# Optimization experiments

Hardware: AMD Instinct MI355X
Metric: run time of the kernel (lower is better)

Reference implementation:

```python
import jax, jax.numpy as jnp
import numpy as np

EPS = 1e-7   # keras.backend.epsilon() added before log in ctc_batch_cost
NEG = -1e30  # log-space 'zero'

B, T, C, L = 256, 1024, 96, 64


def setup_inputs() -> dict:
    key = jax.random.key(0)
    k1, k2 = jax.random.split(key)
    y_true = jax.random.randint(k1, (B, L), 0, C - 1, dtype=jnp.int32)  # labels in [0, C-2], blank = C-1
    y_pred = jax.random.uniform(k2, (B, T, C), dtype=jnp.float32)
    y_pred = y_pred / jnp.sum(y_pred, axis=-1, keepdims=True)  # valid softmax-like probabilities
    return {"y_true": y_true, "y_pred": y_pred}


def _ctc_loss(y_pred, y_true):
    # Faithful re-implementation of keras.backend.ctc_batch_cost with
    # input_length = T and label_length = L for every batch row.
    b, t, c = y_pred.shape
    l = y_true.shape[1]
    blank = c - 1
    s = 2 * l + 1  # extended label length (blanks interleaved)

    logp = jnp.log(y_pred + EPS)  # [B, T, C]

    # extended label sequence: blank, l0, blank, l1, ..., blank
    ext = jnp.full((b, s), blank, dtype=y_true.dtype).at[:, 1::2].set(y_true)  # [B, S]

    # emission log-probs per (t, b, s)
    lp = jnp.take_along_axis(logp, jnp.broadcast_to(ext[:, None, :], (b, t, s)), axis=2)  # [B, T, S]
    lp = jnp.transpose(lp, (1, 0, 2))  # [T, B, S]

    # skip transition s-2 -> s allowed iff ext[s] != blank and ext[s] != ext[s-2]
    ext_m2 = jnp.pad(ext, ((0, 0), (2, 0)), constant_values=-1)[:, :s]
    skip_ok = (ext != blank) & (ext != ext_m2)  # [B, S]

    alpha0 = jnp.full((b, s), NEG, dtype=logp.dtype)
    alpha0 = alpha0.at[:, 0].set(lp[0, :, 0]).at[:, 1].set(lp[0, :, 1])

    def step(alpha, lp_t):
        a1 = jnp.pad(alpha, ((0, 0), (1, 0)), constant_values=NEG)[:, :s]
        a2 = jnp.pad(alpha, ((0, 0), (2, 0)), constant_values=NEG)[:, :s]
        a2 = jnp.where(skip_ok, a2, NEG)
        new = jax.nn.logsumexp(jnp.stack([alpha, a1, a2]), axis=0) + lp_t
        return new, None

    alpha, _ = jax.lax.scan(step, alpha0, lp[1:])

    loss = -jax.nn.logsumexp(jnp.stack([alpha[:, s - 1], alpha[:, s - 2]]), axis=0)
    return loss[:, None]  # [B, 1], matching ctc_batch_cost


def reference(y_true, y_pred):
    return _ctc_loss(y_pred, y_true)
```

## Files before the change

kernel.cpp:

```cpp
#include <hip/hip_runtime.h>
#include <cstdint>


constexpr int BB = 256;
constexpr int TT = 1024;
constexpr int CC = 96;
constexpr int LL = 64;
#define EPSF 1e-7f

__device__ __forceinline__ float wf_shr1_f(float v) {
  int r = __builtin_amdgcn_update_dpp(0, __float_as_int(v), 0x138 , 0xF, 0xF, false);
  return __int_as_float(r);
}

template <int CTRL>
__device__ __forceinline__ float dpp_max(float v) {
  int r = __builtin_amdgcn_update_dpp(__float_as_int(v), __float_as_int(v), CTRL, 0xF, 0xF, false);
  return fmaxf(v, __int_as_float(r));
}

#define GL(dst, ptr, OFF)                                              \
  asm volatile("global_load_dword %0, %1, off offset:" #OFF            \
               : "=&v"(dst) : "v"(ptr))

#define ISSUE(s) do {                                                  \
    GL(Pl[s][0], ql, 0);    GL(Pl[s][1], ql, 384);                     \
    GL(Pl[s][2], ql, 768);  GL(Pl[s][3], ql, 1152);                    \
    GL(Pl[s][4], ql, 1536); GL(Pl[s][5], ql, 1920);                    \
    GL(Pl[s][6], ql, 2304); GL(Pl[s][7], ql, 2688);                    \
    GL(Pb[s][0], qb, 0);    GL(Pb[s][1], qb, 384);                     \
    GL(Pb[s][2], qb, 768);  GL(Pb[s][3], qb, 1152);                    \
    GL(Pb[s][4], qb, 1536); GL(Pb[s][5], qb, 1920);                    \
    GL(Pb[s][6], qb, 2304); GL(Pb[s][7], qb, 2688);                    \
    ql += 8 * CC; qb += 8 * CC;                                        \
  } while (0)

#define WAITN(N) do {                                                  \
    asm volatile("s_waitcnt vmcnt(" #N ")" ::: "memory");              \
    __builtin_amdgcn_sched_barrier(0);                                 \
  } while (0)

#define STEP8(s) do {                                                  \
    _Pragma("unroll")                                                  \
    for (int u = 0; u < 8; ++u) {                                      \
      const float PL  = Pl[s][u] + EPSF;                               \
      const float PB  = Pb[s][u] + EPSF;                               \
      const float a1p = wf_shr1_f(a1);                \
      const float na0 = (a0 + a1p) * PB;              \
      const float na2 = (a2 + a1) * PB;               \
      const float na1 = fmaf(a1p, mskip, a1 + a0) * PL;      \
      a0 = na0; a1 = na1; a2 = na2;                                    \
    }                                                                  \
  } while (0)

#define RESCALE do {                                                   \
    float m = fmaxf(fmaxf(a0, a1), a2);                                \
    m = dpp_max<0x111>(m);                             \
    m = dpp_max<0x112>(m);                             \
    m = dpp_max<0x114>(m);                             \
    m = dpp_max<0x118>(m);                             \
    m = dpp_max<0x142>(m);                           \
    m = dpp_max<0x143>(m);      \
    const int mb = __builtin_amdgcn_readlane(__float_as_int(m), 63);   \
    const int k  = 223 - ((mb >> 23) & 0xFF);        \
    scale += k;                                                        \
    a0 = ldexpf(a0, k); a1 = ldexpf(a1, k); a2 = ldexpf(a2, k);        \
  } while (0)

__global__ void __launch_bounds__(64, 1)
ctc_fwd(const int* __restrict__ y_true, const float* __restrict__ y_pred,
        float* __restrict__ out) {
  const int b    = blockIdx.x;
  const int lane = threadIdx.x;

  const int lab  = y_true[b * LL + lane];
  const int labp = __builtin_amdgcn_update_dpp(-1, lab, 0x138, 0xF, 0xF, false);
  const float mskip = (lane > 0 && lab != labp) ? 1.0f : 0.0f;

  const float* __restrict__ p = y_pred + (size_t)b * (TT * CC);
  const float* ql = p + lab;
  const float* qb = p + (CC - 1);

  float Pl[4][8], Pb[4][8];

  float a0 = (lane == 0) ? 1.0f : 0.0f;
  float a1 = 0.0f;
  float a2 = 0.0f;
  int   scale = 0;

  ISSUE(0); ISSUE(1); ISSUE(2);

#pragma unroll 1
  for (int it = 0; it < 31; ++it) {
    WAITN(32); ISSUE(3); STEP8(0);
    WAITN(32); ISSUE(0); STEP8(1); RESCALE;
    WAITN(32); ISSUE(1); STEP8(2);
    WAITN(32); ISSUE(2); STEP8(3); RESCALE;
  }
  WAITN(32); ISSUE(3); STEP8(0);
  WAITN(32);           STEP8(1); RESCALE;
  WAITN(16);           STEP8(2);
  WAITN(0);            STEP8(3); RESCALE;

  if (lane == 63) {
    const float s = a1 + a2;
    out[b] = 0.693147180559945f * ((float)scale - log2f(s));
  }
}

extern "C" void kernel_launch(void* const* d_in, const int* in_sizes, int n_in,
                              void* d_out, int out_size, void* d_ws, size_t ws_size,
                              hipStream_t stream) {
  (void)in_sizes; (void)n_in; (void)d_ws; (void)ws_size; (void)out_size;
  const int*   y_true = (const int*)d_in[0];
  const float* y_pred = (const float*)d_in[1];
  float*       out    = (float*)d_out;
  ctc_fwd<<<BB, 64, 0, stream>>>(y_true, y_pred, out);
}
```

Baseline: 155.1 us.

## Repack gathered emissions into bf16 coalesced workspace before serial CTC scan

A new parallel pre-pass kernel gathers each lane's label probability and the blank probability per timestep, rounds them to bf16, and writes them in a lane-contiguous layout to the workspace. The serial scan kernel then reads them with wide dwordx4 loads instead of sixteen scattered dword loads per eight steps, shortening the latency-bound per-step memory path. This adds a second launch and a full pass over y_pred, and bf16 rounding reduces probability precision, which may shift the loss slightly. The original kernel is kept as a fallback when the workspace is too small.

```diff
diff --git a/kernel.cpp b/kernel.cpp
--- a/kernel.cpp
+++ b/kernel.cpp
@@ -8,6 +8,8 @@
 constexpr int LL = 64;
 #define EPSF 1e-7f
 
+typedef __attribute__((ext_vector_type(4))) int i32x4;
+
 __device__ __forceinline__ float wf_shr1_f(float v) {
   int r = __builtin_amdgcn_update_dpp(0, __float_as_int(v), 0x138 , 0xF, 0xF, false);
   return __int_as_float(r);
@@ -19,32 +21,74 @@
   return fmaxf(v, __int_as_float(r));
 }
 
-#define GL(dst, ptr, OFF)                                              \
-  asm volatile("global_load_dword %0, %1, off offset:" #OFF            \
+__device__ __forceinline__ unsigned f2bf(float f) {
+  unsigned x = __float_as_uint(f);
+  return (x + 0x7fffu + ((x >> 16) & 1u)) >> 16;
+}
+
+__global__ void __launch_bounds__(256)
+ctc_repack(const int* __restrict__ y_true, const float* __restrict__ y_pred,
+           unsigned* __restrict__ Lout , ushort* __restrict__ Bout) {
+  __shared__ alignas(16) float tile[64 * CC];
+  __shared__ int labs[64];
+  const int blk = blockIdx.x;
+  const int b   = blk >> 4;
+  const int t0  = (blk & 15) * 64;
+  const int tid = threadIdx.x;
+
+  if (tid < 64) labs[tid] = y_true[b * LL + tid];
+  const float* src = y_pred + ((size_t)b * TT + t0) * CC;
+#pragma unroll
+  for (int j = 0; j < 6; ++j)
+    reinterpret_cast<float4*>(tile)[j * 256 + tid] =
+        reinterpret_cast<const float4*>(src)[j * 256 + tid];
+  __syncthreads();
+
+  const int i   = tid & 63;
+  const int gp  = tid >> 6;
+  const int lab = labs[i];
+#pragma unroll
+  for (int k = 0; k < 2; ++k) {
+    const int gl = gp * 2 + k;
+    unsigned o0, o1, o2, o3;
+    {
+      unsigned a, c;
+      a = f2bf(tile[(gl * 8 + 0) * CC + lab]); c = f2bf(tile[(gl * 8 + 1) * CC + lab]); o0 = a | (c << 16);
+      a = f2bf(tile[(gl * 8 + 2) * CC + lab]); c = f2bf(tile[(gl * 8 + 3) * CC + lab]); o1 = a | (c << 16);
+      a = f2bf(tile[(gl * 8 + 4) * CC + lab]); c = f2bf(tile[(gl * 8 + 5) * CC + lab]); o2 = a | (c << 16);
+      a = f2bf(tile[(gl * 8 + 6) * CC + lab]); c = f2bf(tile[(gl * 8 + 7) * CC + lab]); o3 = a | (c << 16);
+    }
+    const int g = b * 128 + (t0 >> 3) + gl;
+    reinterpret_cast<uint4*>(Lout)[(size_t)g * 64 + i] = make_uint4(o0, o1, o2, o3);
+  }
+  if (tid < 64) Bout[(size_t)b * TT + t0 + tid] = (ushort)f2bf(tile[tid * CC + (CC - 1)]);
+}
+
+#define GLX4(dst, ptr, OFF)                                            \
+  asm volatile("global_load_dwordx4 %0, %1, off offset:" #OFF          \
                : "=&v"(dst) : "v"(ptr))
-
-#define ISSUE(s) do {                                                  \
-    GL(Pl[s][0], ql, 0);    GL(Pl[s][1], ql, 384);                     \
-    GL(Pl[s][2], ql, 768);  GL(Pl[s][3], ql, 1152);                    \
-    GL(Pl[s][4], ql, 1536); GL(Pl[s][5], ql, 1920);                    \
-    GL(Pl[s][6], ql, 2304); GL(Pl[s][7], ql, 2688);                    \
-    GL(Pb[s][0], qb, 0);    GL(Pb[s][1], qb, 384);                     \
-    GL(Pb[s][2], qb, 768);  GL(Pb[s][3], qb, 1152);                    \
-    GL(Pb[s][4], qb, 1536); GL(Pb[s][5], qb, 1920);                    \
-    GL(Pb[s][6], qb, 2304); GL(Pb[s][7], qb, 2688);                    \
-    ql += 8 * CC; qb += 8 * CC;                                        \
-  } while (0)
 
 #define WAITN(N) do {                                                  \
     asm volatile("s_waitcnt vmcnt(" #N ")" ::: "memory");              \
     __builtin_amdgcn_sched_barrier(0);                                 \
   } while (0)
 
+#define ISSUE(s, OFF, BOFF) do {                                       \
+    GLX4(Lv[s], ql, OFF);                                              \
+    GLX4(Bv[s], qb, BOFF);                                             \
+  } while (0)
+
+#define ADV do { ql += 4096; qb += 64; } while (0)
+
 #define STEP8(s) do {                                                  \
     _Pragma("unroll")                                                  \
     for (int u = 0; u < 8; ++u) {                                      \
-      const float PL  = Pl[s][u] + EPSF;                               \
-      const float PB  = Pb[s][u] + EPSF;                               \
+      const int ld = Lv[s][u >> 1];                                    \
+      const int bd = Bv[s][u >> 1];                                    \
+      const int li = (u & 1) ? (ld & 0xffff0000) : (ld << 16);         \
+      const int bi = (u & 1) ? (bd & 0xffff0000) : (bd << 16);         \
+      const float PL  = __int_as_float(li) + EPSF;                     \
+      const float PB  = __int_as_float(bi) + EPSF;                     \
       const float a1p = wf_shr1_f(a1);                \
       const float na0 = (a0 + a1p) * PB;              \
       const float na2 = (a2 + a1) * PB;               \
@@ -55,16 +99,81 @@
 
 #define RESCALE do {                                                   \
     float m = fmaxf(fmaxf(a0, a1), a2);                                \
-    m = dpp_max<0x111>(m);                             \
-    m = dpp_max<0x112>(m);                             \
-    m = dpp_max<0x114>(m);                             \
-    m = dpp_max<0x118>(m);                             \
-    m = dpp_max<0x142>(m);                           \
-    m = dpp_max<0x143>(m);      \
+    m = dpp_max<0x111>(m); m = dpp_max<0x112>(m);                      \
+    m = dpp_max<0x114>(m); m = dpp_max<0x118>(m);                      \
+    m = dpp_max<0x142>(m); m = dpp_max<0x143>(m);                      \
     const int mb = __builtin_amdgcn_readlane(__float_as_int(m), 63);   \
     const int k  = 223 - ((mb >> 23) & 0xFF);        \
     scale += k;                                                        \
     a0 = ldexpf(a0, k); a1 = ldexpf(a1, k); a2 = ldexpf(a2, k);        \
+  } while (0)
+
+__global__ void __launch_bounds__(64, 1)
+ctc_scan(const int* __restrict__ y_true, const unsigned* __restrict__ Lin,
+         const ushort* __restrict__ Bin, float* __restrict__ out) {
+  const int b    = blockIdx.x;
+  const int lane = threadIdx.x;
+
+  const int lab  = y_true[b * LL + lane];
+  const int labp = __builtin_amdgcn_update_dpp(-1, lab, 0x138, 0xF, 0xF, false);
+  const float mskip = (lane > 0 && lab != labp) ? 1.0f : 0.0f;
+
+  const char* ql = (const char*)Lin + (size_t)b * 131072 + lane * 16;
+  const char* qb = (const char*)Bin + (size_t)b * 2048;
+
+  i32x4 Lv[4], Bv[4];
+  float a0 = (lane == 0) ? 1.0f : 0.0f;
+  float a1 = 0.0f, a2 = 0.0f;
+  int scale = 0;
+
+  ISSUE(0, 0, 0); ISSUE(1, 1024, 16); ISSUE(2, 2048, 32);
+
+#pragma unroll 1
+  for (int it = 0; it < 31; ++it) {
+    WAITN(4); ISSUE(3, 3072, 48); STEP8(0);
+    ADV;
+    WAITN(4); ISSUE(0, 0, 0);     STEP8(1); RESCALE;
+    WAITN(4); ISSUE(1, 1024, 16); STEP8(2);
+    WAITN(4); ISSUE(2, 2048, 32); STEP8(3); RESCALE;
+  }
+  WAITN(4); ISSUE(3, 3072, 48); STEP8(0);
+  WAITN(4);                      STEP8(1); RESCALE;
+  WAITN(2);                      STEP8(2);
+  WAITN(0);                      STEP8(3); RESCALE;
+
+  if (lane == 63) {
+    const float s = a1 + a2;
+    out[b] = 0.693147180559945f * ((float)scale - log2f(s));
+  }
+}
+
+#define GL(dst, ptr, OFF)                                              \
+  asm volatile("global_load_dword %0, %1, off offset:" #OFF            \
+               : "=&v"(dst) : "v"(ptr))
+
+#define FISSUE(s) do {                                                 \
+    GL(Pl[s][0], fql, 0);    GL(Pl[s][1], fql, 384);                   \
+    GL(Pl[s][2], fql, 768);  GL(Pl[s][3], fql, 1152);                  \
+    GL(Pl[s][4], fql, 1536); GL(Pl[s][5], fql, 1920);                  \
+    GL(Pl[s][6], fql, 2304); GL(Pl[s][7], fql, 2688);                  \
+    GL(Pb[s][0], fqb, 0);    GL(Pb[s][1], fqb, 384);                   \
+    GL(Pb[s][2], fqb, 768);  GL(Pb[s][3], fqb, 1152);                  \
+    GL(Pb[s][4], fqb, 1536); GL(Pb[s][5], fqb, 1920);                  \
+    GL(Pb[s][6], fqb, 2304); GL(Pb[s][7], fqb, 2688);                  \
+    fql += 8 * CC; fqb += 8 * CC;                                      \
+  } while (0)
+
+#define FSTEP8(s) do {                                                 \
+    _Pragma("unroll")                                                  \
+    for (int u = 0; u < 8; ++u) {                                      \
+      const float PL  = Pl[s][u] + EPSF;                               \
+      const float PB  = Pb[s][u] + EPSF;                               \
+      const float a1p = wf_shr1_f(a1);                                 \
+      const float na0 = (a0 + a1p) * PB;                               \
+      const float na2 = (a2 + a1) * PB;                                \
+      const float na1 = fmaf(a1p, mskip, a1 + a0) * PL;                \
+      a0 = na0; a1 = na1; a2 = na2;                                    \
+    }                                                                  \
   } while (0)
 
 __global__ void __launch_bounds__(64, 1)
@@ -72,36 +181,28 @@
         float* __restrict__ out) {
   const int b    = blockIdx.x;
   const int lane = threadIdx.x;
-
   const int lab  = y_true[b * LL + lane];
   const int labp = __builtin_amdgcn_update_dpp(-1, lab, 0x138, 0xF, 0xF, false);
   const float mskip = (lane > 0 && lab != labp) ? 1.0f : 0.0f;
-
   const float* __restrict__ p = y_pred + (size_t)b * (TT * CC);
-  const float* ql = p + lab;
-  const float* qb = p + (CC - 1);
-
+  const float* fql = p + lab;
+  const float* fqb = p + (CC - 1);
   float Pl[4][8], Pb[4][8];
-
   float a0 = (lane == 0) ? 1.0f : 0.0f;
-  float a1 = 0.0f;
-  float a2 = 0.0f;
-  int   scale = 0;
-
-  ISSUE(0); ISSUE(1); ISSUE(2);
-
+  float a1 = 0.0f, a2 = 0.0f;
+  int scale = 0;
+  FISSUE(0); FISSUE(1); FISSUE(2);
 #pragma unroll 1
   for (int it = 0; it < 31; ++it) {
-    WAITN(32); ISSUE(3); STEP8(0);
-    WAITN(32); ISSUE(0); STEP8(1); RESCALE;
-    WAITN(32); ISSUE(1); STEP8(2);
-    WAITN(32); ISSUE(2); STEP8(3); RESCALE;
-  }
-  WAITN(32); ISSUE(3); STEP8(0);
-  WAITN(32);           STEP8(1); RESCALE;
-  WAITN(16);           STEP8(2);
-  WAITN(0);            STEP8(3); RESCALE;
-
+    WAITN(32); FISSUE(3); FSTEP8(0);
+    WAITN(32); FISSUE(0); FSTEP8(1); RESCALE;
+    WAITN(32); FISSUE(1); FSTEP8(2);
+    WAITN(32); FISSUE(2); FSTEP8(3); RESCALE;
+  }
+  WAITN(32); FISSUE(3); FSTEP8(0);
+  WAITN(32);            FSTEP8(1); RESCALE;
+  WAITN(16);            FSTEP8(2);
+  WAITN(0);             FSTEP8(3); RESCALE;
   if (lane == 63) {
     const float s = a1 + a2;
     out[b] = 0.693147180559945f * ((float)scale - log2f(s));
@@ -111,9 +212,19 @@
 extern "C" void kernel_launch(void* const* d_in, const int* in_sizes, int n_in,
                               void* d_out, int out_size, void* d_ws, size_t ws_size,
                               hipStream_t stream) {
-  (void)in_sizes; (void)n_in; (void)d_ws; (void)ws_size; (void)out_size;
+  (void)in_sizes; (void)n_in; (void)out_size;
   const int*   y_true = (const int*)d_in[0];
   const float* y_pred = (const float*)d_in[1];
   float*       out    = (float*)d_out;
-  ctc_fwd<<<BB, 64, 0, stream>>>(y_true, y_pred, out);
-}
+
+  const size_t l_bytes = (size_t)BB * 128 * 64 * 16;
+  const size_t b_bytes = (size_t)BB * TT * 2;
+  if (ws_size >= l_bytes + b_bytes) {
+    unsigned* L = (unsigned*)d_ws;
+    ushort*   Bk = (ushort*)((char*)d_ws + l_bytes);
+    ctc_repack<<<BB * 16, 256, 0, stream>>>(y_true, y_pred, L, Bk);
+    ctc_scan<<<BB, 64, 0, stream>>>(y_true, L, Bk, out);
+  } else {
+    ctc_fwd<<<BB, 64, 0, stream>>>(y_true, y_pred, out);
+  }
+}
```

Measured after the change: 180.3 us. 16.2% more time.
